# Optimization experiments

Measured on AMD Instinct MI355X. Metric: run time of the kernel, lower is better.

## Reference

```python
import jax, jax.numpy as jnp
import numpy as np

B, I, O, D = 8, 16, 16, 512
BASIS = 5

def setup_inputs() -> dict:
    key = jax.random.key(0)
    k1, k2, k3 = jax.random.split(key, 3)
    x = jax.random.normal(k1, (B, I, D), dtype=jnp.float32)
    fan_in = BASIS * I  # kaiming_uniform(a=sqrt(5)) on (O, 5I, 1, 1) -> bound = 1/sqrt(fan_in)
    bound = 1.0 / np.sqrt(fan_in)
    weight = jax.random.uniform(k2, (O, BASIS * I), dtype=jnp.float32, minval=-bound, maxval=bound)
    bias = jax.random.uniform(k3, (O,), dtype=jnp.float32, minval=-bound, maxval=bound)
    return {"x": x, "weight": weight, "bias": bias}

def reference(x, weight, bias):
    # x: (B, I, D); weight: (O, 5*I); bias: (O,)
    # Equivariant 1->2 basis ops (normalize=False), fused with the 1x1-conv channel
    # contraction instead of materializing the (B, 5I, D, D) concat:
    #   op1 = diag_embed(x); op2 = row-broadcast(x); op3 = col-broadcast(x);
    #   op4 = diag_embed(sum(x)); op5 = full-broadcast(sum(x))
    b_, i_, d_ = x.shape
    o_ = weight.shape[0]
    w = weight.reshape(o_, BASIS, i_)  # channel layout of the concat: [op1|op2|op3|op4|op5]
    s = x.sum(axis=-1)                                     # (B, I)
    y1 = jnp.einsum('oi,bid->bod', w[:, 0], x)             # diagonal term
    y2 = jnp.einsum('oi,bid->bod', w[:, 1], x)             # row broadcast term
    y3 = jnp.einsum('oi,bid->bod', w[:, 2], x)             # col broadcast term
    y4 = jnp.einsum('oi,bi->bo', w[:, 3], s)               # sum on diagonal
    y5 = jnp.einsum('oi,bi->bo', w[:, 4], s)               # sum everywhere
    out = y2[..., :, None] + y3[..., None, :] + y5[..., None, None]  # (B, O, D, D)
    diag = y1 + y4[..., None]                              # (B, O, D)
    out = out + jnp.eye(d_, dtype=x.dtype) * diag[..., :, None]
    return out + bias[None, :, None, None]
```

## Files before the change

kernel.cpp:

```cpp
#include <hip/hip_runtime.h>

#define NB 8
#define NI 16
#define NO 16
#define ND 512
#define ROWS 32
#define RT   (ND / ROWS)

typedef float f32x4 __attribute__((ext_vector_type(4)));

__global__ __launch_bounds__(256) void leq_fused(
    const float* __restrict__ x, const float* __restrict__ weight,
    const float* __restrict__ bias, f32x4* __restrict__ out)
{
    const int blk = blockIdx.x;
    const int rt  = blk & (RT - 1);
    const int bo  = blk >> 4;
    const int b   = bo >> 4;
    const int o   = bo & 15;
    const int t   = threadIdx.x;

    __shared__ __align__(16) float colvS[ND];
    __shared__ __align__(16) float part1[ND];
    __shared__ __align__(16) float part2[ND];
    __shared__ __align__(16) float part3[ND];
    __shared__ float rwS[ROWS], dgS[ROWS];
    __shared__ float red4[4], red5[4];

    const float* wbase = weight + o * (5 * NI);
    const float* xb    = x + b * (NI * ND);
    const float  bia   = bias[o];

    const int half = t >> 7;
    const int fq   = t & 127;

    f32x4 a1 = {0,0,0,0}, a2 = {0,0,0,0}, a3 = {0,0,0,0};
    float p4 = 0.f, p5 = 0.f;

    #pragma unroll
    for (int i2 = 0; i2 < NI / 2; ++i2) {
        const int   i  = i2 * 2 + half;
        const float w0 = wbase[0 * NI + i];
        const float w1 = wbase[1 * NI + i];
        const float w2 = wbase[2 * NI + i];
        const float w3 = wbase[3 * NI + i];
        const float w4 = wbase[4 * NI + i];
        const f32x4 xv = reinterpret_cast<const f32x4*>(xb + i * ND)[fq];
        a1 += w0 * xv;
        a2 += w1 * xv;
        a3 += w2 * xv;
        const float xs = xv.x + xv.y + xv.z + xv.w;
        p4 += w3 * xs; p5 += w4 * xs;
    }

    if (half) {
        reinterpret_cast<f32x4*>(part1)[fq] = a1;
        reinterpret_cast<f32x4*>(part2)[fq] = a2;
        reinterpret_cast<f32x4*>(part3)[fq] = a3;
    }

    #pragma unroll
    for (int off = 32; off > 0; off >>= 1) {
        p4 += __shfl_down(p4, off, 64);
        p5 += __shfl_down(p5, off, 64);
    }
    const int wave = t >> 6, lane = t & 63;
    if (lane == 0) { red4[wave] = p4; red5[wave] = p5; }
    __syncthreads();

    const float y4   = red4[0] + red4[1] + red4[2] + red4[3];
    const float y5   = red5[0] + red5[1] + red5[2] + red5[3];
    const float base = y5 + bia;

    if (half == 0) {
        const f32x4 o1 = reinterpret_cast<const f32x4*>(part1)[fq];
        const f32x4 o2 = reinterpret_cast<const f32x4*>(part2)[fq];
        const f32x4 o3 = reinterpret_cast<const f32x4*>(part3)[fq];
        reinterpret_cast<f32x4*>(colvS)[fq] = a3 + o3;
        if ((fq >> 3) == rt) {
            const int rl4 = (fq & 7) << 2;
            const f32x4 rw = a2 + o2;
            const f32x4 dg = a1 + o1;
            rwS[rl4 + 0] = rw.x + base;
            rwS[rl4 + 1] = rw.y + base;
            rwS[rl4 + 2] = rw.z + base;
            rwS[rl4 + 3] = rw.w + base;
            dgS[rl4 + 0] = dg.x + y4;
            dgS[rl4 + 1] = dg.y + y4;
            dgS[rl4 + 2] = dg.z + y4;
            dgS[rl4 + 3] = dg.w + y4;
        }
    }
    __syncthreads();

    const int   c4    = t & 127;
    const f32x4 cv    = reinterpret_cast<const f32x4*>(colvS)[c4];
    const int   cbase = c4 << 2;
    const int   out_base = bo * (ND * (ND / 4)) + rt * ROWS * (ND / 4);
    const int   rbase = rt * ROWS;

    #pragma unroll
    for (int k = 0; k < 16; ++k) {
        const int rl = (k << 1) + half;
        const float rv = rwS[rl];
        const float dv = dgS[rl];
        const int dcol = (rbase + rl) - cbase;
        f32x4 res;
        res.x = rv + cv.x + ((dcol == 0) ? dv : 0.0f);
        res.y = rv + cv.y + ((dcol == 1) ? dv : 0.0f);
        res.z = rv + cv.z + ((dcol == 2) ? dv : 0.0f);
        res.w = rv + cv.w + ((dcol == 3) ? dv : 0.0f);
        out[out_base + (rl << 7) + c4] = res;
    }
}

extern "C" void kernel_launch(void* const* d_in, const int* in_sizes, int n_in,
                              void* d_out, int out_size, void* d_ws, size_t ws_size,
                              hipStream_t stream) {
    const float* x      = (const float*)d_in[0];
    const float* weight = (const float*)d_in[1];
    const float* bias   = (const float*)d_in[2];

    leq_fused<<<NB * NO * RT, 256, 0, stream>>>(x, weight, bias, (f32x4*)d_out);
}
```

Baseline: 27.73 us.

## Split fused kernel into vector-prep and broadcast-store kernels via workspace

Replaces the single fused kernel, in which every row-chunk block recomputed the full channel contraction for its (b,o) pair, with two kernels. A prep kernel computes the row, column and diagonal vectors once per (b,o) and writes them to workspace. A store kernel reads them back and writes the broadcast output tiles. This removes the 16x redundant contraction work, at the cost of a second launch and a global-memory round trip for the intermediate vectors.

```diff
diff --git a/kernel.cpp b/kernel.cpp
--- a/kernel.cpp
+++ b/kernel.cpp
@@ -4,27 +4,24 @@
 #define NI 16
 #define NO 16
 #define ND 512
-#define ROWS 32
-#define RT   (ND / ROWS)
+#define CHUNK_ROWS 32
+#define NCHUNK (ND / CHUNK_ROWS)
 
 typedef float f32x4 __attribute__((ext_vector_type(4)));
 
-__global__ __launch_bounds__(256) void leq_fused(
+__global__ __launch_bounds__(256) void leq_prep(
     const float* __restrict__ x, const float* __restrict__ weight,
-    const float* __restrict__ bias, f32x4* __restrict__ out)
+    const float* __restrict__ bias, float* __restrict__ rowv,
+    float* __restrict__ colv, float* __restrict__ diagv)
 {
-    const int blk = blockIdx.x;
-    const int rt  = blk & (RT - 1);
-    const int bo  = blk >> 4;
-    const int b   = bo >> 4;
-    const int o   = bo & 15;
-    const int t   = threadIdx.x;
+    const int bo = blockIdx.x;
+    const int b  = bo >> 4;
+    const int o  = bo & 15;
+    const int t  = threadIdx.x;
 
-    __shared__ __align__(16) float colvS[ND];
     __shared__ __align__(16) float part1[ND];
     __shared__ __align__(16) float part2[ND];
     __shared__ __align__(16) float part3[ND];
-    __shared__ float rwS[ROWS], dgS[ROWS];
     __shared__ float red4[4], red5[4];
 
     const float* wbase = weight + o * (5 * NI);
@@ -76,34 +73,41 @@
         const f32x4 o1 = reinterpret_cast<const f32x4*>(part1)[fq];
         const f32x4 o2 = reinterpret_cast<const f32x4*>(part2)[fq];
         const f32x4 o3 = reinterpret_cast<const f32x4*>(part3)[fq];
-        reinterpret_cast<f32x4*>(colvS)[fq] = a3 + o3;
-        if ((fq >> 3) == rt) {
-            const int rl4 = (fq & 7) << 2;
-            const f32x4 rw = a2 + o2;
-            const f32x4 dg = a1 + o1;
-            rwS[rl4 + 0] = rw.x + base;
-            rwS[rl4 + 1] = rw.y + base;
-            rwS[rl4 + 2] = rw.z + base;
-            rwS[rl4 + 3] = rw.w + base;
-            dgS[rl4 + 0] = dg.x + y4;
-            dgS[rl4 + 1] = dg.y + y4;
-            dgS[rl4 + 2] = dg.z + y4;
-            dgS[rl4 + 3] = dg.w + y4;
-        }
+        const f32x4 c3 = a3 + o3;
+        f32x4 rw = a2 + o2;
+        f32x4 dg = a1 + o1;
+        rw += base;
+        dg += y4;
+        reinterpret_cast<f32x4*>(colv  + bo * ND)[fq] = c3;
+        reinterpret_cast<f32x4*>(rowv  + bo * ND)[fq] = rw;
+        reinterpret_cast<f32x4*>(diagv + bo * ND)[fq] = dg;
     }
-    __syncthreads();
+}
 
-    const int   c4    = t & 127;
-    const f32x4 cv    = reinterpret_cast<const f32x4*>(colvS)[c4];
-    const int   cbase = c4 << 2;
-    const int   out_base = bo * (ND * (ND / 4)) + rt * ROWS * (ND / 4);
-    const int   rbase = rt * ROWS;
+__global__ __launch_bounds__(256) void leq_store(
+    const float* __restrict__ rowv, const float* __restrict__ colv,
+    const float* __restrict__ diagv, f32x4* __restrict__ out)
+{
+    const int blk   = blockIdx.x;
+    const int chunk = blk & (NCHUNK - 1);
+    const int bo    = blk >> 4;
+    const int t     = threadIdx.x;
+
+    const int half = t >> 7;
+    const int c4   = t & 127;
+    const int cbase = c4 << 2;
+
+    const f32x4 cv = reinterpret_cast<const f32x4*>(colv + bo * ND)[c4];
+    const int rbase = chunk * CHUNK_ROWS;
+    const float* rv_p = rowv  + bo * ND + rbase;
+    const float* dv_p = diagv + bo * ND + rbase;
+    const int out_base = bo * (ND * (ND / 4)) + rbase * (ND / 4);
 
     #pragma unroll
-    for (int k = 0; k < 16; ++k) {
+    for (int k = 0; k < CHUNK_ROWS / 2; ++k) {
         const int rl = (k << 1) + half;
-        const float rv = rwS[rl];
-        const float dv = dgS[rl];
+        const float rv = rv_p[rl];
+        const float dv = dv_p[rl];
         const int dcol = (rbase + rl) - cbase;
         f32x4 res;
         res.x = rv + cv.x + ((dcol == 0) ? dv : 0.0f);
@@ -121,5 +125,11 @@
     const float* weight = (const float*)d_in[1];
     const float* bias   = (const float*)d_in[2];
 
-    leq_fused<<<NB * NO * RT, 256, 0, stream>>>(x, weight, bias, (f32x4*)d_out);
+    float* ws    = (float*)d_ws;
+    float* rowv  = ws;
+    float* colv  = ws + NB * NO * ND;
+    float* diagv = ws + 2 * NB * NO * ND;
+
+    leq_prep<<<NB * NO, 256, 0, stream>>>(x, weight, bias, rowv, colv, diagv);
+    leq_store<<<NB * NO * NCHUNK, 256, 0, stream>>>(rowv, colv, diagv, (f32x4*)d_out);
 }
```

Measured after the change: 31.18 us. 1.12x slower.
